# Kernel optimization log

Measured on AMD Instinct MI355X. Metric: run time of the kernel, lower is better.

Reference implementation:

```python
import jax, jax.numpy as jnp
import numpy as np

B = 8192
D_S, D_W, D_P, D_E, D_C, D_Z = 1024, 1024, 512, 1024, 512, 512
H_P = 2 * D_P          # particle hidden_dim default
RANK = D_W // 4        # low-rank A factor
EPS = 1e-5             # torch LayerNorm default eps


def _ln(x, g, b):
    m = jnp.mean(x, axis=-1, keepdims=True)
    v = jnp.var(x, axis=-1, keepdims=True)
    return (x - m) * jax.lax.rsqrt(v + EPS) * g + b


def setup_inputs() -> dict:
    key = jax.random.key(0)
    ks = iter(jax.random.split(key, 48))
    def randn(shape, scale=1.0):
        return jax.random.normal(next(ks), shape, dtype=jnp.float32) * scale
    def lin(dout, din):  # torch Linear: W [out,in], b [out]
        s = 1.0 / np.sqrt(din)
        return randn((dout, din), s), randn((dout,), s)
    inp = {}
    inp["s_prev"] = randn((B, D_S))
    inp["w_prev"] = randn((B, D_W))
    inp["p_prev"] = randn((B, D_P))
    inp["e_t"] = randn((B, D_E))
    inp["c_t"] = randn((B, D_C))
    d_in = D_S + D_E + D_C
    # fusion_net: Linear -> LN -> ReLU -> Linear
    inp["fw1"], inp["fb1"] = lin(2 * D_Z, d_in)
    inp["fln_g"] = jnp.ones((2 * D_Z,), jnp.float32)
    inp["fln_b"] = jnp.zeros((2 * D_Z,), jnp.float32)
    inp["fw2"], inp["fb2"] = lin(D_Z, 2 * D_Z)
    # wave subsystem
    inp["A_diag"] = jnp.zeros((D_W,), jnp.float32)
    inp["A_U"] = randn((D_W, RANK), 0.01)
    inp["A_V"] = randn((D_W, RANK), 0.01)
    inp["amod_w"], inp["amod_b"] = lin(D_W, D_C)
    inp["bnet_w"], inp["bnet_b"] = lin(D_W, D_C + D_Z)
    # particle subsystem phi
    inp["pw1"], inp["pb1"] = lin(H_P, D_P + D_Z + D_C)
    inp["pln_g"] = jnp.ones((H_P,), jnp.float32)
    inp["pln_b"] = jnp.zeros((H_P,), jnp.float32)
    inp["pw2"], inp["pb2"] = lin(H_P // 2, H_P)
    inp["pw3"], inp["pb3"] = lin(D_P, H_P // 2)
    # gate + mixing projections + output norm
    inp["gw"], inp["gb"] = lin(D_S, d_in)
    inp["uw"] = randn((D_S, D_W), 1.0 / np.sqrt(D_W))
    inp["up"] = randn((D_S, D_P), 1.0 / np.sqrt(D_P))
    inp["oln_g"] = jnp.ones((D_S,), jnp.float32)
    inp["oln_b"] = jnp.zeros((D_S,), jnp.float32)
    return inp


def reference(s_prev, w_prev, p_prev, e_t, c_t,
              fw1, fb1, fln_g, fln_b, fw2, fb2,
              A_diag, A_U, A_V, amod_w, amod_b, bnet_w, bnet_b,
              pw1, pb1, pln_g, pln_b, pw2, pb2, pw3, pb3,
              gw, gb, uw, up, oln_g, oln_b):
    # fusion: z_t = Linear(ReLU(LN(Linear([s||e||c]))))
    fin = jnp.concatenate([s_prev, e_t, c_t], axis=-1)      # [B, d_s+d_e+d_c]
    h = jax.nn.relu(_ln(fin @ fw1.T + fb1, fln_g, fln_b))
    z_t = h @ fw2.T + fb2                                   # [B, d_z]
    # wave: A = (diag(tanh(A_diag)*0.9) + A_U A_V^T) * mod[None,:]
    # so (A w)[b,i] = sum_j A_base[i,j] * (mod*w)[b,j] -> (mod*w) @ A_base^T
    A_base = jnp.diag(jnp.tanh(A_diag) * 0.9) + A_U @ A_V.T  # [d_w, d_w]
    mod = jnp.tanh(c_t @ amod_w.T + amod_b)                  # [B, d_w]
    w_linear = (mod * w_prev) @ A_base.T
    b_in = jnp.concatenate([c_t, z_t], axis=-1)
    w_t = w_linear + b_in @ bnet_w.T + bnet_b                # [B, d_w]
    # particle: p_t = p_prev + tanh(MLP([p||z||c]))
    pin = jnp.concatenate([p_prev, z_t, c_t], axis=-1)
    h1 = jax.nn.relu(_ln(pin @ pw1.T + pb1, pln_g, pln_b))
    h2 = jax.nn.relu(h1 @ pw2.T + pb2)
    p_t = p_prev + jnp.tanh(h2 @ pw3.T + pb3)                # [B, d_p]
    # gated mixing
    g_t = jax.nn.sigmoid(fin @ gw.T + gb)                    # [B, d_s]
    s_t = s_prev + g_t * (p_t @ up.T) + (1.0 - g_t) * (w_t @ uw.T)
    s_t = _ln(s_t, oln_g, oln_b)
    return (s_t, w_t, p_t)
```

## Files before the change

### kernel.cpp

```cpp
#include <hip/hip_runtime.h>
#include <math.h>

typedef unsigned short u16;
typedef __attribute__((ext_vector_type(8))) short short8;
typedef __attribute__((ext_vector_type(4))) float f32x4;

#define AS1C(p) ((const __attribute__((address_space(1))) void*)(p))
#define AS3(p)  ((__attribute__((address_space(3))) void*)(p))

static __device__ __forceinline__ float b2f(u16 h) {
    union { unsigned u; float f; } c; c.u = ((unsigned)h) << 16; return c.f;
}
static __device__ __forceinline__ u16 f2b(float f) {
    union { float f; unsigned u; } c; c.f = f;
    unsigned r = c.u + 0x7FFFu + ((c.u >> 16) & 1u);
    return (u16)(r >> 16);
}

#define EP_NONE     0
#define EP_RELU     1
#define EP_SIGMOID  2
#define EP_TANH_MUL 3
#define EP_TANH_ADD 4
#define EP_DIAG     5

struct GDesc {
    const u16* A;
    const u16* W;
    const float* bias;
    const float* auxf;
    u16* outb;
    float* outf;
    int lda, ldd, N, K, ep, nbm;
};

struct GArgs { GDesc d0, d1, d2; int s1, s2; };

__global__ __launch_bounds__(256)
void gemm_multi(GArgs ga)
{
    __shared__ __align__(16) u16 As[128 * 64];
    __shared__ __align__(16) u16 Bs[128 * 64];

    const int bid = (int)blockIdx.x;
    GDesc dd = (bid < ga.s1) ? ga.d0 : ((bid < ga.s2) ? ga.d1 : ga.d2);
    const int b = bid - ((bid < ga.s1) ? 0 : ((bid < ga.s2) ? ga.s1 : ga.s2));

    const int tid  = threadIdx.x;
    const int bm   = b % dd.nbm;
    const int bn   = b / dd.nbm;
    const int lane = tid & 63;
    const int wave = tid >> 6;
    const int wr   = wave >> 1;
    const int wc   = wave & 1;

    const int srow = tid >> 3;
    const int scol = (tid & 7) * 8;

    const int lda = dd.lda, K = dd.K, N = dd.N, ldd = dd.ldd;

    const u16* Ab = dd.A + (size_t)(bm * 128 + srow) * lda + scol;
    const u16* Wb = dd.W + (size_t)(bn * 128 + srow) * K + scol;
    u16* Asl = As + srow * 64 + scol;
    u16* Bsl = Bs + srow * 64 + scol;

    f32x4 acc[4][4];
#pragma unroll
    for (int m = 0; m < 4; ++m)
#pragma unroll
        for (int n = 0; n < 4; ++n) acc[m][n] = (f32x4){0.f, 0.f, 0.f, 0.f};

    const u16* ArdBase = As + ((wr * 64) + (lane & 15)) * 64 + (lane >> 4) * 8;
    const u16* BrdBase = Bs + ((wc * 64) + (lane & 15)) * 64 + (lane >> 4) * 8;

    for (int k0 = 0; k0 < K; k0 += 64) {
#pragma unroll
        for (int i = 0; i < 4; ++i) {
            __builtin_amdgcn_global_load_lds(AS1C(Ab + (size_t)(i * 32) * lda + k0),
                                             AS3(Asl + i * 32 * 64), 16, 0, 0);
            __builtin_amdgcn_global_load_lds(AS1C(Wb + (size_t)(i * 32) * K + k0),
                                             AS3(Bsl + i * 32 * 64), 16, 0, 0);
        }
        __syncthreads();
#pragma unroll
        for (int kk = 0; kk < 64; kk += 32) {
            short8 a[4], bb[4];
#pragma unroll
            for (int m = 0; m < 4; ++m) a[m] = *(const short8*)(ArdBase + m * 16 * 64 + kk);
#pragma unroll
            for (int n = 0; n < 4; ++n) bb[n] = *(const short8*)(BrdBase + n * 16 * 64 + kk);
#pragma unroll
            for (int m = 0; m < 4; ++m)
#pragma unroll
                for (int n = 0; n < 4; ++n)
                    acc[m][n] = __builtin_amdgcn_mfma_f32_16x16x32_bf16(a[m], bb[n], acc[m][n], 0, 0, 0);
        }
        __syncthreads();
    }

    const int rbase = bm * 128 + wr * 64 + (lane >> 4) * 4;
    const int cbase = bn * 128 + wc * 64 + (lane & 15);
    const int ep = dd.ep;
#pragma unroll
    for (int n = 0; n < 4; ++n) {
        const int C = cbase + n * 16;
        const float bv = dd.bias ? dd.bias[C] : 0.f;
#pragma unroll
        for (int m = 0; m < 4; ++m) {
            const int R0 = rbase + m * 16;
#pragma unroll
            for (int j = 0; j < 4; ++j) {
                const int R = R0 + j;
                float v = acc[m][n][j] + bv;
                if (ep == EP_RELU)          v = fmaxf(v, 0.f);
                else if (ep == EP_SIGMOID)  v = 1.f / (1.f + expf(-v));
                else if (ep == EP_TANH_MUL) v = tanhf(v) * dd.auxf[(size_t)R * N + C];
                else if (ep == EP_TANH_ADD) v = dd.auxf[(size_t)R * N + C] + tanhf(v);
                else if (ep == EP_DIAG)     { if (R == C) v += 0.9f * tanhf(dd.auxf[R]); }
                dd.outb[(size_t)R * ldd + C] = f2b(v);
                if (dd.outf) dd.outf[(size_t)R * N + C] = v;
            }
        }
    }
}

template<bool RELU>
__global__ __launch_bounds__(256)
void ln1024(u16* __restrict__ X, const float* __restrict__ gam, const float* __restrict__ bet)
{
    const int row = blockIdx.x;
    u16* xp = X + (size_t)row * 1024 + threadIdx.x * 4;
    u16 loc[4];
    *(uint2*)loc = *(const uint2*)xp;
    float x0 = b2f(loc[0]), x1 = b2f(loc[1]), x2 = b2f(loc[2]), x3 = b2f(loc[3]);
    float s = x0 + x1 + x2 + x3;
    float q = x0 * x0 + x1 * x1 + x2 * x2 + x3 * x3;
#pragma unroll
    for (int off = 32; off; off >>= 1) { s += __shfl_xor(s, off); q += __shfl_xor(q, off); }
    __shared__ float sm[8];
    const int wave = threadIdx.x >> 6, lane = threadIdx.x & 63;
    if (lane == 0) { sm[wave] = s; sm[4 + wave] = q; }
    __syncthreads();
    s = sm[0] + sm[1] + sm[2] + sm[3];
    q = sm[4] + sm[5] + sm[6] + sm[7];
    const float mean = s * (1.f / 1024.f);
    const float var  = q * (1.f / 1024.f) - mean * mean;
    const float inv  = rsqrtf(var + 1e-5f);
    const int cb = threadIdx.x * 4;
#pragma unroll
    for (int j = 0; j < 4; ++j) {
        float y = (b2f(loc[j]) - mean) * inv * gam[cb + j] + bet[cb + j];
        if (RELU) y = fmaxf(y, 0.f);
        loc[j] = f2b(y);
    }
    *(uint2*)xp = *(uint2*)loc;
}

__global__ __launch_bounds__(256)
void mix_ln(const float* __restrict__ sp, const u16* __restrict__ gt,
            const u16* __restrict__ pm, const u16* __restrict__ wm,
            const float* __restrict__ og, const float* __restrict__ ob,
            float* __restrict__ out)
{
    const int row = blockIdx.x;
    const size_t base = (size_t)row * 1024 + threadIdx.x * 4;
    float4 lsp = *(const float4*)(sp + base);
    u16 lg[4], lp[4], lw[4];
    *(uint2*)lg = *(const uint2*)(gt + base);
    *(uint2*)lp = *(const uint2*)(pm + base);
    *(uint2*)lw = *(const uint2*)(wm + base);
    float x[4];
    const float* lspp = (const float*)&lsp;
#pragma unroll
    for (int j = 0; j < 4; ++j) {
        float g = b2f(lg[j]);
        x[j] = lspp[j] + g * b2f(lp[j]) + (1.f - g) * b2f(lw[j]);
    }
    float s = x[0] + x[1] + x[2] + x[3];
    float q = x[0]*x[0] + x[1]*x[1] + x[2]*x[2] + x[3]*x[3];
#pragma unroll
    for (int off = 32; off; off >>= 1) { s += __shfl_xor(s, off); q += __shfl_xor(q, off); }
    __shared__ float sm[8];
    const int wave = threadIdx.x >> 6, lane = threadIdx.x & 63;
    if (lane == 0) { sm[wave] = s; sm[4 + wave] = q; }
    __syncthreads();
    s = sm[0] + sm[1] + sm[2] + sm[3];
    q = sm[4] + sm[5] + sm[6] + sm[7];
    const float mean = s * (1.f / 1024.f);
    const float var  = q * (1.f / 1024.f) - mean * mean;
    const float inv  = rsqrtf(var + 1e-5f);
    const int cb = threadIdx.x * 4;
    float4 o;
    float* op = (float*)&o;
#pragma unroll
    for (int j = 0; j < 4; ++j)
        op[j] = (x[j] - mean) * inv * og[cb + j] + ob[cb + j];
    *(float4*)(out + base) = o;
}

struct CDesc { const void* src; u16* dst; int srcCols8; int dstStride; int dstOff; unsigned end; int isbf16; };
struct CArgs { CDesc d[16]; unsigned total; };

__global__ __launch_bounds__(256)
void multi_copy(CArgs ca)
{
    const unsigned idx = blockIdx.x * 256 + threadIdx.x;
    if (idx >= ca.total) return;
    int i = 0; unsigned start = 0;
    while (idx >= ca.d[i].end) { start = ca.d[i].end; ++i; }
    const CDesc cd = ca.d[i];
    const unsigned local = idx - start;
    const int r = local / cd.srcCols8;
    const int c = local % cd.srcCols8;
    u16 o[8];
    if (cd.isbf16) {
        *(uint4*)o = *(const uint4*)((const u16*)cd.src + ((size_t)r * cd.srcCols8 + c) * 8);
    } else {
        const float* s = (const float*)cd.src + ((size_t)r * cd.srcCols8 + c) * 8;
        const float4 a = *(const float4*)s;
        const float4 bq = *(const float4*)(s + 4);
        const float* ap = (const float*)&a;
        const float* bp = (const float*)&bq;
#pragma unroll
        for (int j = 0; j < 4; ++j) { o[j] = f2b(ap[j]); o[4 + j] = f2b(bp[j]); }
    }
    *(uint4*)(cd.dst + (size_t)r * cd.dstStride + cd.dstOff + (size_t)c * 8) = *(uint4*)o;
}

extern "C" void kernel_launch(void* const* d_in, const int* in_sizes, int n_in,
                              void* d_out, int out_size, void* d_ws, size_t ws_size,
                              hipStream_t stream)
{
    const float* s_prev = (const float*)d_in[0];
    const float* w_prev = (const float*)d_in[1];
    const float* p_prev = (const float*)d_in[2];
    const float* e_t    = (const float*)d_in[3];
    const float* c_t    = (const float*)d_in[4];
    const float* fw1    = (const float*)d_in[5];
    const float* fb1    = (const float*)d_in[6];
    const float* fln_g  = (const float*)d_in[7];
    const float* fln_b  = (const float*)d_in[8];
    const float* fw2    = (const float*)d_in[9];
    const float* fb2    = (const float*)d_in[10];
    const float* A_diag = (const float*)d_in[11];
    const float* A_U    = (const float*)d_in[12];
    const float* A_V    = (const float*)d_in[13];
    const float* amod_w = (const float*)d_in[14];
    const float* amod_b = (const float*)d_in[15];
    const float* bnet_w = (const float*)d_in[16];
    const float* bnet_b = (const float*)d_in[17];
    const float* pw1    = (const float*)d_in[18];
    const float* pb1    = (const float*)d_in[19];
    const float* pln_g  = (const float*)d_in[20];
    const float* pln_b  = (const float*)d_in[21];
    const float* pw2    = (const float*)d_in[22];
    const float* pb2    = (const float*)d_in[23];
    const float* pw3    = (const float*)d_in[24];
    const float* pb3    = (const float*)d_in[25];
    const float* gw     = (const float*)d_in[26];
    const float* gb     = (const float*)d_in[27];
    const float* uw     = (const float*)d_in[28];
    const float* up     = (const float*)d_in[29];
    const float* oln_g  = (const float*)d_in[30];
    const float* oln_b  = (const float*)d_in[31];

    float* out_s = (float*)d_out;
    float* out_w = out_s + (size_t)8192 * 1024;
    float* out_p = out_w + (size_t)8192 * 1024;

    u16* ws = (u16*)d_ws;
    u16* FIN  = ws;
    u16* W_bf = ws + 12582912;
    u16* H    = ws + 20971520;
    u16* P_bf = H;
    u16* Z    = ws + 29360128;
    u16* G    = ws + 33554432;
    u16* ACAT = ws + 41943040;
    u16* PM   = ACAT;
    u16* WM   = ACAT + 8388608;
    u16* WCAT = ws + 58720256;
    u16* wb   = ws + 60817408;
    u16* fw1b  = wb;
    u16* gwb   = wb + 2621440;
    u16* fw2b  = wb + 5242880;
    u16* amodb = wb + 5767168;
    u16* pw1b  = wb + 6291456;
    u16* pw2b  = wb + 7864320;
    u16* pw3b  = wb + 8388608;
    u16* uwb   = wb + 8650752;
    u16* upb   = wb + 9699328;
    u16* AUb   = wb + 10223616;
    u16* AVb   = wb + 10485760;

    const dim3 blk(256);

    {
        CArgs ca; unsigned cum = 0; int nd = 0;
        auto push = [&](const void* src, u16* dst, int cols8, int stride, int off,
                        int rows, int isbf) {
            cum += (unsigned)rows * cols8;
            ca.d[nd++] = CDesc{src, dst, cols8, stride, off, cum, isbf};
        };
        push(fw1,    fw1b,  320, 2560, 0,    1024, 0);
        push(gw,     gwb,   320, 2560, 0,    1024, 0);
        push(fw2,    fw2b,  128, 1024, 0,    512,  0);
        push(amod_w, amodb, 64,  512,  0,    1024, 0);
        push(pw1,    pw1b,  192, 1536, 0,    1024, 0);
        push(pw2,    pw2b,  128, 1024, 0,    512,  0);
        push(pw3,    pw3b,  64,  512,  0,    512,  0);
        push(uw,     uwb,   128, 1024, 0,    1024, 0);
        push(up,     upb,   64,  512,  0,    1024, 0);
        push(A_U,    AUb,   32,  256,  0,    1024, 0);
        push(A_V,    AVb,   32,  256,  0,    1024, 0);
        push(s_prev, FIN,   128, 2560, 0,    8192, 0);
        push(e_t,    FIN,   128, 2560, 1024, 8192, 0);
        push(c_t,    FIN,   64,  2560, 2048, 8192, 0);
        push(c_t,    ACAT,  64,  2048, 1024, 8192, 0);
        push(bnet_w, WCAT,  128, 2048, 1024, 1024, 0);
        ca.total = cum;
        multi_copy<<<dim3((cum + 255) / 256), blk, 0, stream>>>(ca);
    }

    {
        GArgs ga;
        ga.d0 = GDesc{FIN, fw1b, fb1, nullptr, H, nullptr, 2560, 1024, 1024, 2560, EP_NONE,    64};
        ga.d1 = GDesc{FIN, gwb,  gb,  nullptr, G, nullptr, 2560, 1024, 1024, 2560, EP_SIGMOID, 64};
        ga.d2 = ga.d1; ga.s1 = 512; ga.s2 = 1024;
        gemm_multi<<<dim3(1024), blk, 0, stream>>>(ga);
    }
    ln1024<true><<<8192, blk, 0, stream>>>(H, fln_g, fln_b);

    {
        GArgs ga;
        ga.d0 = GDesc{H,          fw2b,  fb2,    nullptr, Z,    nullptr, 1024, 512,  512,  1024, EP_NONE,     64};
        ga.d1 = GDesc{FIN + 2048, amodb, amod_b, w_prev,  ACAT, nullptr, 2560, 2048, 1024, 512,  EP_TANH_MUL, 64};
        ga.d2 = GDesc{AUb,        AVb,   nullptr, A_diag, WCAT, nullptr, 256,  2048, 1024, 256,  EP_DIAG,     8};
        ga.s1 = 256; ga.s2 = 768;
        gemm_multi<<<dim3(832), blk, 0, stream>>>(ga);
    }

    {
        CArgs ca; unsigned cum = 0; int nd = 0;
        auto push = [&](const void* src, u16* dst, int cols8, int stride, int off,
                        int rows, int isbf) {
            cum += (unsigned)rows * cols8;
            ca.d[nd++] = CDesc{src, dst, cols8, stride, off, cum, isbf};
        };
        push(p_prev, FIN,  64, 1536, 0,    8192, 0);
        push(Z,      FIN,  64, 1536, 512,  8192, 1);
        push(c_t,    FIN,  64, 1536, 1024, 8192, 0);
        push(Z,      ACAT, 64, 2048, 1536, 8192, 1);
        ca.total = cum;
        multi_copy<<<dim3((cum + 255) / 256), blk, 0, stream>>>(ca);
    }

    {
        GArgs ga;
        ga.d0 = GDesc{ACAT, WCAT, bnet_b, nullptr, W_bf, out_w, 2048, 1024, 1024, 2048, EP_NONE, 64};
        ga.d1 = GDesc{FIN,  pw1b, pb1,    nullptr, H,    nullptr, 1536, 1024, 1024, 1536, EP_NONE, 64};
        ga.d2 = ga.d1; ga.s1 = 512; ga.s2 = 1024;
        gemm_multi<<<dim3(1024), blk, 0, stream>>>(ga);
    }
    ln1024<true><<<8192, blk, 0, stream>>>(H, pln_g, pln_b);

    {
        GArgs ga;
        ga.d0 = GDesc{H,    pw2b, pb2,    nullptr, Z,  nullptr, 1024, 512,  512,  1024, EP_RELU, 64};
        ga.d1 = GDesc{W_bf, uwb,  nullptr, nullptr, WM, nullptr, 1024, 1024, 1024, 1024, EP_NONE, 64};
        ga.d2 = ga.d1; ga.s1 = 256; ga.s2 = 768;
        gemm_multi<<<dim3(768), blk, 0, stream>>>(ga);
    }

    {
        GArgs ga;
        ga.d0 = GDesc{Z, pw3b, pb3, p_prev, P_bf, out_p, 512, 512, 512, 512, EP_TANH_ADD, 64};
        ga.d1 = ga.d0; ga.d2 = ga.d0; ga.s1 = 256; ga.s2 = 256;
        gemm_multi<<<dim3(256), blk, 0, stream>>>(ga);
    }

    {
        GArgs ga;
        ga.d0 = GDesc{P_bf, upb, nullptr, nullptr, PM, nullptr, 512, 1024, 1024, 512, EP_NONE, 64};
        ga.d1 = ga.d0; ga.d2 = ga.d0; ga.s1 = 512; ga.s2 = 512;
        gemm_multi<<<dim3(512), blk, 0, stream>>>(ga);
    }

    mix_ln<<<8192, blk, 0, stream>>>(s_prev, G, PM, WM, oln_g, oln_b, out_s);
}
```

Before: 534.7 us.

## Replace 128x128 GEMM with 256x256-tile double-buffered swizzled MFMA kernel

The multi-descriptor GEMM moves from 128x128 tiles with 256 threads and a single LDS buffer to 256x256 tiles with 512 threads (8 waves). The new kernel double-buffers global-to-LDS loads so the next K-tile loads while MFMAs run, and XOR-swizzles LDS columns to avoid bank conflicts. It also interleaves fragment loads with MFMA groups under raised wave priority. This aims to improve operand reuse and hide load latency. The cost is far fewer blocks per launch (as few as 64), which can leave many CUs idle on the smaller GEMMs, plus 128KB of LDS per block that limits occupancy.

```diff
diff --git a/kernel.cpp b/kernel.cpp
--- a/kernel.cpp
+++ b/kernel.cpp
@@ -36,77 +36,142 @@
 
 struct GArgs { GDesc d0, d1, d2; int s1, s2; };
 
-__global__ __launch_bounds__(256)
-void gemm_multi(GArgs ga)
+__global__ __launch_bounds__(512, 2)
+void gemm256(GArgs ga)
 {
-    __shared__ __align__(16) u16 As[128 * 64];
-    __shared__ __align__(16) u16 Bs[128 * 64];
+    __shared__ __align__(16) u16 LDS[65536];
 
     const int bid = (int)blockIdx.x;
     GDesc dd = (bid < ga.s1) ? ga.d0 : ((bid < ga.s2) ? ga.d1 : ga.d2);
     const int b = bid - ((bid < ga.s1) ? 0 : ((bid < ga.s2) ? ga.s1 : ga.s2));
 
     const int tid  = threadIdx.x;
-    const int bm   = b % dd.nbm;
-    const int bn   = b / dd.nbm;
     const int lane = tid & 63;
-    const int wave = tid >> 6;
-    const int wr   = wave >> 1;
-    const int wc   = wave & 1;
-
-    const int srow = tid >> 3;
-    const int scol = (tid & 7) * 8;
-
+    const int wid  = tid >> 6;
+    const int wr   = wid >> 2;
+    const int wc   = wid & 3;
+
+    const int bm = b % dd.nbm;
+    const int bn = b / dd.nbm;
     const int lda = dd.lda, K = dd.K, N = dd.N, ldd = dd.ldd;
 
-    const u16* Ab = dd.A + (size_t)(bm * 128 + srow) * lda + scol;
-    const u16* Wb = dd.W + (size_t)(bn * 128 + srow) * K + scol;
-    u16* Asl = As + srow * 64 + scol;
-    u16* Bsl = Bs + srow * 64 + scol;
-
-    f32x4 acc[4][4];
-#pragma unroll
-    for (int m = 0; m < 4; ++m)
+    const int srow  = tid >> 3;
+    const int sslot = tid & 7;
+    const int sgcol = (sslot ^ (srow & 7)) * 8;
+    const u16* Abase = dd.A + (size_t)(bm * 256 + srow) * lda + sgcol;
+    const u16* Wbase = dd.W + (size_t)(bn * 256 + srow) * K + sgcol;
+    const int ldst = tid * 8;
+
+    f32x4 acc[8][4];
+#pragma unroll
+    for (int m = 0; m < 8; ++m)
 #pragma unroll
         for (int n = 0; n < 4; ++n) acc[m][n] = (f32x4){0.f, 0.f, 0.f, 0.f};
 
-    const u16* ArdBase = As + ((wr * 64) + (lane & 15)) * 64 + (lane >> 4) * 8;
-    const u16* BrdBase = Bs + ((wc * 64) + (lane & 15)) * 64 + (lane >> 4) * 8;
-
-    for (int k0 = 0; k0 < K; k0 += 64) {
-#pragma unroll
-        for (int i = 0; i < 4; ++i) {
-            __builtin_amdgcn_global_load_lds(AS1C(Ab + (size_t)(i * 32) * lda + k0),
-                                             AS3(Asl + i * 32 * 64), 16, 0, 0);
-            __builtin_amdgcn_global_load_lds(AS1C(Wb + (size_t)(i * 32) * K + k0),
-                                             AS3(Bsl + i * 32 * 64), 16, 0, 0);
-        }
-        __syncthreads();
-#pragma unroll
-        for (int kk = 0; kk < 64; kk += 32) {
-            short8 a[4], bb[4];
-#pragma unroll
-            for (int m = 0; m < 4; ++m) a[m] = *(const short8*)(ArdBase + m * 16 * 64 + kk);
-#pragma unroll
-            for (int n = 0; n < 4; ++n) bb[n] = *(const short8*)(BrdBase + n * 16 * 64 + kk);
-#pragma unroll
-            for (int m = 0; m < 4; ++m)
-#pragma unroll
-                for (int n = 0; n < 4; ++n)
-                    acc[m][n] = __builtin_amdgcn_mfma_f32_16x16x32_bf16(a[m], bb[n], acc[m][n], 0, 0, 0);
-        }
-        __syncthreads();
-    }
-
-    const int rbase = bm * 128 + wr * 64 + (lane >> 4) * 4;
-    const int cbase = bn * 128 + wc * 64 + (lane & 15);
+    const int nkt = K >> 6;
+
+#define STAGE(bufi, kt)                                                          \
+    {                                                                            \
+        const int k0_ = (kt) << 6;                                               \
+        u16* al_ = &LDS[(bufi) * 32768 + ldst];                                  \
+        u16* bl_ = &LDS[(bufi) * 32768 + 16384 + ldst];                          \
+        _Pragma("unroll")                                                        \
+        for (int j = 0; j < 4; ++j)                                              \
+            __builtin_amdgcn_global_load_lds(AS1C(Abase + (size_t)j * 64 * lda + k0_), \
+                                             AS3(al_ + j * 4096), 16, 0, 0);     \
+        _Pragma("unroll")                                                        \
+        for (int j = 0; j < 4; ++j)                                              \
+            __builtin_amdgcn_global_load_lds(AS1C(Wbase + (size_t)j * 64 * K + k0_),   \
+                                             AS3(bl_ + j * 4096), 16, 0, 0);     \
+    }
+
+#define WAITBAR()                                                                \
+    {                                                                            \
+        asm volatile("s_waitcnt vmcnt(0)" ::: "memory");                         \
+        __builtin_amdgcn_sched_barrier(0);                                       \
+        __builtin_amdgcn_s_barrier();                                            \
+        __builtin_amdgcn_sched_barrier(0);                                       \
+    }
+
+    const int swz = (lane & 7) << 4;
+    const int cnat = (lane >> 4) << 4;
+
+    short8 AF0[4][2], AF1[4][2], BF[2][2];
+
+#define LDA_SET(AF, rh, Al)                                                      \
+    {                                                                            \
+        const int rb_ = wr * 128 + (rh) * 64 + (lane & 15);                      \
+        _Pragma("unroll")                                                        \
+        for (int mm = 0; mm < 4; ++mm) {                                         \
+            const u16* rp_ = (Al) + (rb_ + mm * 16) * 64;                        \
+            _Pragma("unroll")                                                    \
+            for (int ks = 0; ks < 2; ++ks)                                       \
+                AF[mm][ks] = *(const short8*)(rp_ + ((((ks << 6) | cnat) ^ swz) >> 1)); \
+        }                                                                        \
+    }
+
+#define LDB_SET(ch, Bl)                                                          \
+    {                                                                            \
+        const int rb_ = wc * 64 + (ch) * 32 + (lane & 15);                       \
+        _Pragma("unroll")                                                        \
+        for (int nn = 0; nn < 2; ++nn) {                                         \
+            const u16* rp_ = (Bl) + (rb_ + nn * 16) * 64;                        \
+            _Pragma("unroll")                                                    \
+            for (int ks = 0; ks < 2; ++ks)                                       \
+                BF[nn][ks] = *(const short8*)(rp_ + ((((ks << 6) | cnat) ^ swz) >> 1)); \
+        }                                                                        \
+    }
+
+#define QMFMA(AF, rh, ch)                                                        \
+    {                                                                            \
+        __builtin_amdgcn_s_setprio(1);                                           \
+        _Pragma("unroll")                                                        \
+        for (int mm = 0; mm < 4; ++mm)                                           \
+            _Pragma("unroll")                                                    \
+            for (int nn = 0; nn < 2; ++nn)                                       \
+                _Pragma("unroll")                                                \
+                for (int ks = 0; ks < 2; ++ks)                                   \
+                    acc[(rh) * 4 + mm][(ch) * 2 + nn] =                          \
+                        __builtin_amdgcn_mfma_f32_16x16x32_bf16(                 \
+                            AF[mm][ks], BF[nn][ks], acc[(rh) * 4 + mm][(ch) * 2 + nn], 0, 0, 0); \
+        __builtin_amdgcn_s_setprio(0);                                           \
+    }
+
+    STAGE(0, 0);
+    WAITBAR();
+
+    int buf = 0;
+    for (int kt = 0; kt < nkt; ++kt) {
+        if (kt + 1 < nkt) STAGE(buf ^ 1, kt + 1);
+        const u16* Al = &LDS[buf * 32768];
+        const u16* Bl = Al + 16384;
+        LDA_SET(AF0, 0, Al);
+        LDB_SET(0, Bl);
+        QMFMA(AF0, 0, 0);
+        LDA_SET(AF1, 1, Al);
+        QMFMA(AF1, 1, 0);
+        LDB_SET(1, Bl);
+        QMFMA(AF1, 1, 1);
+        QMFMA(AF0, 0, 1);
+        WAITBAR();
+        buf ^= 1;
+    }
+
+#undef STAGE
+#undef WAITBAR
+#undef LDA_SET
+#undef LDB_SET
+#undef QMFMA
+
+    const int rbase = bm * 256 + wr * 128 + (lane >> 4) * 4;
+    const int cbase = bn * 256 + wc * 64 + (lane & 15);
     const int ep = dd.ep;
 #pragma unroll
     for (int n = 0; n < 4; ++n) {
         const int C = cbase + n * 16;
         const float bv = dd.bias ? dd.bias[C] : 0.f;
 #pragma unroll
-        for (int m = 0; m < 4; ++m) {
+        for (int m = 0; m < 8; ++m) {
             const int R0 = rbase + m * 16;
 #pragma unroll
             for (int j = 0; j < 4; ++j) {
@@ -293,6 +358,7 @@
     u16* AVb   = wb + 10485760;
 
     const dim3 blk(256);
+    const dim3 blk512(512);
 
     {
         CArgs ca; unsigned cum = 0; int nd = 0;
@@ -323,20 +389,20 @@
 
     {
         GArgs ga;
-        ga.d0 = GDesc{FIN, fw1b, fb1, nullptr, H, nullptr, 2560, 1024, 1024, 2560, EP_NONE,    64};
-        ga.d1 = GDesc{FIN, gwb,  gb,  nullptr, G, nullptr, 2560, 1024, 1024, 2560, EP_SIGMOID, 64};
-        ga.d2 = ga.d1; ga.s1 = 512; ga.s2 = 1024;
-        gemm_multi<<<dim3(1024), blk, 0, stream>>>(ga);
+        ga.d0 = GDesc{FIN, fw1b, fb1, nullptr, H, nullptr, 2560, 1024, 1024, 2560, EP_NONE,    32};
+        ga.d1 = GDesc{FIN, gwb,  gb,  nullptr, G, nullptr, 2560, 1024, 1024, 2560, EP_SIGMOID, 32};
+        ga.d2 = ga.d1; ga.s1 = 128; ga.s2 = 256;
+        gemm256<<<dim3(256), blk512, 0, stream>>>(ga);
     }
     ln1024<true><<<8192, blk, 0, stream>>>(H, fln_g, fln_b);
 
     {
         GArgs ga;
-        ga.d0 = GDesc{H,          fw2b,  fb2,    nullptr, Z,    nullptr, 1024, 512,  512,  1024, EP_NONE,     64};
-        ga.d1 = GDesc{FIN + 2048, amodb, amod_b, w_prev,  ACAT, nullptr, 2560, 2048, 1024, 512,  EP_TANH_MUL, 64};
-        ga.d2 = GDesc{AUb,        AVb,   nullptr, A_diag, WCAT, nullptr, 256,  2048, 1024, 256,  EP_DIAG,     8};
-        ga.s1 = 256; ga.s2 = 768;
-        gemm_multi<<<dim3(832), blk, 0, stream>>>(ga);
+        ga.d0 = GDesc{H,          fw2b,  fb2,     nullptr, Z,    nullptr, 1024, 512,  512,  1024, EP_NONE,     32};
+        ga.d1 = GDesc{FIN + 2048, amodb, amod_b,  w_prev,  ACAT, nullptr, 2560, 2048, 1024, 512,  EP_TANH_MUL, 32};
+        ga.d2 = GDesc{AUb,        AVb,   nullptr, A_diag,  WCAT, nullptr, 256,  2048, 1024, 256,  EP_DIAG,     4};
+        ga.s1 = 64; ga.s2 = 192;
+        gemm256<<<dim3(208), blk512, 0, stream>>>(ga);
     }
 
     {
@@ -356,33 +422,33 @@
 
     {
         GArgs ga;
-        ga.d0 = GDesc{ACAT, WCAT, bnet_b, nullptr, W_bf, out_w, 2048, 1024, 1024, 2048, EP_NONE, 64};
-        ga.d1 = GDesc{FIN,  pw1b, pb1,    nullptr, H,    nullptr, 1536, 1024, 1024, 1536, EP_NONE, 64};
-        ga.d2 = ga.d1; ga.s1 = 512; ga.s2 = 1024;
-        gemm_multi<<<dim3(1024), blk, 0, stream>>>(ga);
+        ga.d0 = GDesc{ACAT, WCAT, bnet_b, nullptr, W_bf, out_w,   2048, 1024, 1024, 2048, EP_NONE, 32};
+        ga.d1 = GDesc{FIN,  pw1b, pb1,    nullptr, H,    nullptr, 1536, 1024, 1024, 1536, EP_NONE, 32};
+        ga.d2 = ga.d1; ga.s1 = 128; ga.s2 = 256;
+        gemm256<<<dim3(256), blk512, 0, stream>>>(ga);
     }
     ln1024<true><<<8192, blk, 0, stream>>>(H, pln_g, pln_b);
 
     {
         GArgs ga;
-        ga.d0 = GDesc{H,    pw2b, pb2,    nullptr, Z,  nullptr, 1024, 512,  512,  1024, EP_RELU, 64};
-        ga.d1 = GDesc{W_bf, uwb,  nullptr, nullptr, WM, nullptr, 1024, 1024, 1024, 1024, EP_NONE, 64};
-        ga.d2 = ga.d1; ga.s1 = 256; ga.s2 = 768;
-        gemm_multi<<<dim3(768), blk, 0, stream>>>(ga);
-    }
-
-    {
-        GArgs ga;
-        ga.d0 = GDesc{Z, pw3b, pb3, p_prev, P_bf, out_p, 512, 512, 512, 512, EP_TANH_ADD, 64};
-        ga.d1 = ga.d0; ga.d2 = ga.d0; ga.s1 = 256; ga.s2 = 256;
-        gemm_multi<<<dim3(256), blk, 0, stream>>>(ga);
-    }
-
-    {
-        GArgs ga;
-        ga.d0 = GDesc{P_bf, upb, nullptr, nullptr, PM, nullptr, 512, 1024, 1024, 512, EP_NONE, 64};
-        ga.d1 = ga.d0; ga.d2 = ga.d0; ga.s1 = 512; ga.s2 = 512;
-        gemm_multi<<<dim3(512), blk, 0, stream>>>(ga);
+        ga.d0 = GDesc{H,    pw2b, pb2,     nullptr, Z,  nullptr, 1024, 512,  512,  1024, EP_RELU, 32};
+        ga.d1 = GDesc{W_bf, uwb,  nullptr, nullptr, WM, nullptr, 1024, 1024, 1024, 1024, EP_NONE, 32};
+        ga.d2 = ga.d1; ga.s1 = 64; ga.s2 = 192;
+        gemm256<<<dim3(192), blk512, 0, stream>>>(ga);
+    }
+
+    {
+        GArgs ga;
+        ga.d0 = GDesc{Z, pw3b, pb3, p_prev, P_bf, out_p, 512, 512, 512, 512, EP_TANH_ADD, 32};
+        ga.d1 = ga.d0; ga.d2 = ga.d0; ga.s1 = 64; ga.s2 = 64;
+        gemm256<<<dim3(64), blk512, 0, stream>>>(ga);
+    }
+
+    {
+        GArgs ga;
+        ga.d0 = GDesc{P_bf, upb, nullptr, nullptr, PM, nullptr, 512, 1024, 1024, 512, EP_NONE, 32};
+        ga.d1 = ga.d0; ga.d2 = ga.d0; ga.s1 = 128; ga.s2 = 128;
+        gemm256<<<dim3(128), blk512, 0, stream>>>(ga);
     }
 
     mix_ln<<<8192, blk, 0, stream>>>(s_prev, G, PM, WM, oln_g, oln_b, out_s);
```

Measured after the change: 556.3 us. +4.0%, slower.

## Rewrite GEMM as 256x128-tile multi-buffered pipelined kernel with swizzled LDS

Applied to the files above, without the earlier changes.

Replaces the 128x128, 256-thread GEMM with a 512-thread kernel on 256x128 tiles. A is double-buffered and the weight operand uses a 4-deep ring of LDS slots, so global-to-LDS prefetch overlaps the MFMA work instead of synchronising twice per k-step. LDS columns are XOR-swizzled to avoid bank conflicts, and MFMA sections run at raised wave priority. The 128 KB LDS footprint and larger tiles lower occupancy and halve grid sizes, which risks poorer load balance on the smaller GEMMs.

```diff
diff --git a/kernel.cpp b/kernel.cpp
--- a/kernel.cpp
+++ b/kernel.cpp
@@ -36,33 +36,32 @@
 
 struct GArgs { GDesc d0, d1, d2; int s1, s2; };
 
-__global__ __launch_bounds__(256)
-void gemm_multi(GArgs ga)
+__global__ __launch_bounds__(512, 2)
+void gemm_p(GArgs ga)
 {
-    __shared__ __align__(16) u16 As[128 * 64];
-    __shared__ __align__(16) u16 Bs[128 * 64];
+    __shared__ __align__(16) u16 LDS[65536];
 
     const int bid = (int)blockIdx.x;
     GDesc dd = (bid < ga.s1) ? ga.d0 : ((bid < ga.s2) ? ga.d1 : ga.d2);
     const int b = bid - ((bid < ga.s1) ? 0 : ((bid < ga.s2) ? ga.s1 : ga.s2));
 
     const int tid  = threadIdx.x;
-    const int bm   = b % dd.nbm;
-    const int bn   = b / dd.nbm;
     const int lane = tid & 63;
-    const int wave = tid >> 6;
-    const int wr   = wave >> 1;
-    const int wc   = wave & 1;
-
-    const int srow = tid >> 3;
-    const int scol = (tid & 7) * 8;
-
+    const int wid  = tid >> 6;
+    const int wr   = wid >> 1;
+    const int wc   = wid & 1;
+
+    const int bm = b % dd.nbm;
+    const int bn = b / dd.nbm;
     const int lda = dd.lda, K = dd.K, N = dd.N, ldd = dd.ldd;
-
-    const u16* Ab = dd.A + (size_t)(bm * 128 + srow) * lda + scol;
-    const u16* Wb = dd.W + (size_t)(bn * 128 + srow) * K + scol;
-    u16* Asl = As + srow * 64 + scol;
-    u16* Bsl = Bs + srow * 64 + scol;
+    const int nkt = K >> 6;
+
+    const int srow  = tid >> 3;
+    const int sslot = tid & 7;
+    const int sgcol = (sslot ^ (srow & 7)) * 8;
+    const u16* Ag = dd.A + (size_t)(bm * 256 + srow) * lda + sgcol;
+    const u16* Wg = dd.W + (size_t)(bn * 128 + srow) * K + sgcol;
+    const int ldst = tid * 8;
 
     f32x4 acc[4][4];
 #pragma unroll
@@ -70,35 +69,89 @@
 #pragma unroll
         for (int n = 0; n < 4; ++n) acc[m][n] = (f32x4){0.f, 0.f, 0.f, 0.f};
 
-    const u16* ArdBase = As + ((wr * 64) + (lane & 15)) * 64 + (lane >> 4) * 8;
-    const u16* BrdBase = Bs + ((wc * 64) + (lane & 15)) * 64 + (lane >> 4) * 8;
-
-    for (int k0 = 0; k0 < K; k0 += 64) {
-#pragma unroll
-        for (int i = 0; i < 4; ++i) {
-            __builtin_amdgcn_global_load_lds(AS1C(Ab + (size_t)(i * 32) * lda + k0),
-                                             AS3(Asl + i * 32 * 64), 16, 0, 0);
-            __builtin_amdgcn_global_load_lds(AS1C(Wb + (size_t)(i * 32) * K + k0),
-                                             AS3(Bsl + i * 32 * 64), 16, 0, 0);
+#define STAGE_A(bufi, kt)                                                        \
+    {                                                                            \
+        const int k0_ = (kt) << 6;                                               \
+        u16* d_ = &LDS[(bufi) * 16384 + ldst];                                   \
+        _Pragma("unroll")                                                        \
+        for (int j = 0; j < 4; ++j)                                              \
+            __builtin_amdgcn_global_load_lds(AS1C(Ag + (size_t)(j * 64) * lda + k0_), \
+                                             AS3(d_ + j * 4096), 16, 0, 0);      \
+    }
+#define STAGE_B(sloti, kt)                                                       \
+    {                                                                            \
+        const int k0_ = (kt) << 6;                                               \
+        u16* d_ = &LDS[32768 + (sloti) * 8192 + ldst];                           \
+        _Pragma("unroll")                                                        \
+        for (int j = 0; j < 2; ++j)                                              \
+            __builtin_amdgcn_global_load_lds(AS1C(Wg + (size_t)(j * 64) * K + k0_),   \
+                                             AS3(d_ + j * 4096), 16, 0, 0);      \
+    }
+
+    const int swz  = (lane & 7) << 4;
+    const int cnat = (lane >> 4) << 4;
+
+    STAGE_A(0, 0);
+    __builtin_amdgcn_sched_barrier(0);
+    STAGE_B(0, 0);
+    STAGE_B(1, 1);
+    STAGE_B(2, 2);
+    __builtin_amdgcn_sched_barrier(0);
+    asm volatile("s_waitcnt vmcnt(4)" ::: "memory");
+    __builtin_amdgcn_sched_barrier(0);
+    __builtin_amdgcn_s_barrier();
+    __builtin_amdgcn_sched_barrier(0);
+
+    for (int kt = 0; kt < nkt; ++kt) {
+        const int abuf = kt & 1;
+        const int ka = (kt + 1 < nkt) ? kt + 1 : nkt - 1;
+        const int kb = (kt + 3 < nkt) ? kt + 3 : nkt - 1;
+        STAGE_A(abuf ^ 1, ka);
+        __builtin_amdgcn_sched_barrier(0);
+        STAGE_B((kt + 3) & 3, kb);
+        __builtin_amdgcn_sched_barrier(0);
+
+        const u16* Al = &LDS[abuf * 16384];
+        const u16* Bl = &LDS[32768 + (kt & 3) * 8192];
+
+        short8 af[4][2], bf[4][2];
+#pragma unroll
+        for (int m = 0; m < 4; ++m) {
+            const u16* rp = Al + (wr * 64 + m * 16 + (lane & 15)) * 64;
+#pragma unroll
+            for (int ks = 0; ks < 2; ++ks)
+                af[m][ks] = *(const short8*)(rp + ((((ks << 6) | cnat) ^ swz) >> 1));
         }
-        __syncthreads();
-#pragma unroll
-        for (int kk = 0; kk < 64; kk += 32) {
-            short8 a[4], bb[4];
-#pragma unroll
-            for (int m = 0; m < 4; ++m) a[m] = *(const short8*)(ArdBase + m * 16 * 64 + kk);
-#pragma unroll
-            for (int n = 0; n < 4; ++n) bb[n] = *(const short8*)(BrdBase + n * 16 * 64 + kk);
-#pragma unroll
-            for (int m = 0; m < 4; ++m)
-#pragma unroll
-                for (int n = 0; n < 4; ++n)
-                    acc[m][n] = __builtin_amdgcn_mfma_f32_16x16x32_bf16(a[m], bb[n], acc[m][n], 0, 0, 0);
+#pragma unroll
+        for (int n = 0; n < 4; ++n) {
+            const u16* rp = Bl + (wc * 64 + n * 16 + (lane & 15)) * 64;
+#pragma unroll
+            for (int ks = 0; ks < 2; ++ks)
+                bf[n][ks] = *(const short8*)(rp + ((((ks << 6) | cnat) ^ swz) >> 1));
         }
-        __syncthreads();
-    }
-
-    const int rbase = bm * 128 + wr * 64 + (lane >> 4) * 4;
+
+        __builtin_amdgcn_s_setprio(1);
+#pragma unroll
+        for (int m = 0; m < 4; ++m)
+#pragma unroll
+            for (int n = 0; n < 4; ++n)
+#pragma unroll
+                for (int ks = 0; ks < 2; ++ks)
+                    acc[m][n] = __builtin_amdgcn_mfma_f32_16x16x32_bf16(
+                        af[m][ks], bf[n][ks], acc[m][n], 0, 0, 0);
+        __builtin_amdgcn_s_setprio(0);
+
+        __builtin_amdgcn_sched_barrier(0);
+        asm volatile("s_waitcnt vmcnt(2)" ::: "memory");
+        __builtin_amdgcn_sched_barrier(0);
+        __builtin_amdgcn_s_barrier();
+        __builtin_amdgcn_sched_barrier(0);
+    }
+
+#undef STAGE_A
+#undef STAGE_B
+
+    const int rbase = bm * 256 + wr * 64 + (lane >> 4) * 4;
     const int cbase = bn * 128 + wc * 64 + (lane & 15);
     const int ep = dd.ep;
 #pragma unroll
@@ -293,6 +346,7 @@
     u16* AVb   = wb + 10485760;
 
     const dim3 blk(256);
+    const dim3 blk512(512);
 
     {
         CArgs ca; unsigned cum = 0; int nd = 0;
@@ -323,20 +377,20 @@
 
     {
         GArgs ga;
-        ga.d0 = GDesc{FIN, fw1b, fb1, nullptr, H, nullptr, 2560, 1024, 1024, 2560, EP_NONE,    64};
-        ga.d1 = GDesc{FIN, gwb,  gb,  nullptr, G, nullptr, 2560, 1024, 1024, 2560, EP_SIGMOID, 64};
-        ga.d2 = ga.d1; ga.s1 = 512; ga.s2 = 1024;
-        gemm_multi<<<dim3(1024), blk, 0, stream>>>(ga);
+        ga.d0 = GDesc{FIN, fw1b, fb1, nullptr, H, nullptr, 2560, 1024, 1024, 2560, EP_NONE,    32};
+        ga.d1 = GDesc{FIN, gwb,  gb,  nullptr, G, nullptr, 2560, 1024, 1024, 2560, EP_SIGMOID, 32};
+        ga.d2 = ga.d1; ga.s1 = 256; ga.s2 = 512;
+        gemm_p<<<dim3(512), blk512, 0, stream>>>(ga);
     }
     ln1024<true><<<8192, blk, 0, stream>>>(H, fln_g, fln_b);
 
     {
         GArgs ga;
-        ga.d0 = GDesc{H,          fw2b,  fb2,    nullptr, Z,    nullptr, 1024, 512,  512,  1024, EP_NONE,     64};
-        ga.d1 = GDesc{FIN + 2048, amodb, amod_b, w_prev,  ACAT, nullptr, 2560, 2048, 1024, 512,  EP_TANH_MUL, 64};
-        ga.d2 = GDesc{AUb,        AVb,   nullptr, A_diag, WCAT, nullptr, 256,  2048, 1024, 256,  EP_DIAG,     8};
-        ga.s1 = 256; ga.s2 = 768;
-        gemm_multi<<<dim3(832), blk, 0, stream>>>(ga);
+        ga.d0 = GDesc{H,          fw2b,  fb2,     nullptr, Z,    nullptr, 1024, 512,  512,  1024, EP_NONE,     32};
+        ga.d1 = GDesc{FIN + 2048, amodb, amod_b,  w_prev,  ACAT, nullptr, 2560, 2048, 1024, 512,  EP_TANH_MUL, 32};
+        ga.d2 = GDesc{AUb,        AVb,   nullptr, A_diag,  WCAT, nullptr, 256,  2048, 1024, 256,  EP_DIAG,     4};
+        ga.s1 = 128; ga.s2 = 384;
+        gemm_p<<<dim3(416), blk512, 0, stream>>>(ga);
     }
 
     {
@@ -356,33 +410,33 @@
 
     {
         GArgs ga;
-        ga.d0 = GDesc{ACAT, WCAT, bnet_b, nullptr, W_bf, out_w, 2048, 1024, 1024, 2048, EP_NONE, 64};
-        ga.d1 = GDesc{FIN,  pw1b, pb1,    nullptr, H,    nullptr, 1536, 1024, 1024, 1536, EP_NONE, 64};
-        ga.d2 = ga.d1; ga.s1 = 512; ga.s2 = 1024;
-        gemm_multi<<<dim3(1024), blk, 0, stream>>>(ga);
+        ga.d0 = GDesc{ACAT, WCAT, bnet_b, nullptr, W_bf, out_w,   2048, 1024, 1024, 2048, EP_NONE, 32};
+        ga.d1 = GDesc{FIN,  pw1b, pb1,    nullptr, H,    nullptr, 1536, 1024, 1024, 1536, EP_NONE, 32};
+        ga.d2 = ga.d1; ga.s1 = 256; ga.s2 = 512;
+        gemm_p<<<dim3(512), blk512, 0, stream>>>(ga);
     }
     ln1024<true><<<8192, blk, 0, stream>>>(H, pln_g, pln_b);
 
     {
         GArgs ga;
-        ga.d0 = GDesc{H,    pw2b, pb2,    nullptr, Z,  nullptr, 1024, 512,  512,  1024, EP_RELU, 64};
-        ga.d1 = GDesc{W_bf, uwb,  nullptr, nullptr, WM, nullptr, 1024, 1024, 1024, 1024, EP_NONE, 64};
-        ga.d2 = ga.d1; ga.s1 = 256; ga.s2 = 768;
-        gemm_multi<<<dim3(768), blk, 0, stream>>>(ga);
-    }
-
-    {
-        GArgs ga;
-        ga.d0 = GDesc{Z, pw3b, pb3, p_prev, P_bf, out_p, 512, 512, 512, 512, EP_TANH_ADD, 64};
+        ga.d0 = GDesc{H,    pw2b, pb2,     nullptr, Z,  nullptr, 1024, 512,  512,  1024, EP_RELU, 32};
+        ga.d1 = GDesc{W_bf, uwb,  nullptr, nullptr, WM, nullptr, 1024, 1024, 1024, 1024, EP_NONE, 32};
+        ga.d2 = ga.d1; ga.s1 = 128; ga.s2 = 384;
+        gemm_p<<<dim3(384), blk512, 0, stream>>>(ga);
+    }
+
+    {
+        GArgs ga;
+        ga.d0 = GDesc{Z, pw3b, pb3, p_prev, P_bf, out_p, 512, 512, 512, 512, EP_TANH_ADD, 32};
+        ga.d1 = ga.d0; ga.d2 = ga.d0; ga.s1 = 128; ga.s2 = 128;
+        gemm_p<<<dim3(128), blk512, 0, stream>>>(ga);
+    }
+
+    {
+        GArgs ga;
+        ga.d0 = GDesc{P_bf, upb, nullptr, nullptr, PM, nullptr, 512, 1024, 1024, 512, EP_NONE, 32};
         ga.d1 = ga.d0; ga.d2 = ga.d0; ga.s1 = 256; ga.s2 = 256;
-        gemm_multi<<<dim3(256), blk, 0, stream>>>(ga);
-    }
-
-    {
-        GArgs ga;
-        ga.d0 = GDesc{P_bf, upb, nullptr, nullptr, PM, nullptr, 512, 1024, 1024, 512, EP_NONE, 64};
-        ga.d1 = ga.d0; ga.d2 = ga.d0; ga.s1 = 512; ga.s2 = 512;
-        gemm_multi<<<dim3(512), blk, 0, stream>>>(ga);
+        gemm_p<<<dim3(256), blk512, 0, stream>>>(ga);
     }
 
     mix_ln<<<8192, blk, 0, stream>>>(s_prev, G, PM, WM, oln_g, oln_b, out_s);
```

Measured after the change: 463.0 us. -13.4%, faster.
